# Optimization experiments

Measured on AMD Instinct MI355X. Metric: run time of the kernel, lower is better.

## Reference

```python
import jax, jax.numpy as jnp
import numpy as np

BN_EPS = 1e-5
ITER_N = 5

def _bn(x, gamma, beta, mean, var, axis):
    shape = [1] * x.ndim
    shape[axis] = -1
    r = lambda v: v.reshape(shape)
    return (x - r(mean)) * (r(gamma) / jnp.sqrt(r(var) + BN_EPS)) + r(beta)

def _covpool(x):
    # x: (B, d, M); MPNCOV CovpoolLayer: y = x @ I_hat @ x^T, I_hat = (1/M)I - (1/M^2)11^T
    M = x.shape[-1]
    I_hat = (-1.0 / (M * M)) * jnp.ones((M, M), x.dtype) + (1.0 / M) * jnp.eye(M, dtype=x.dtype)
    return jnp.einsum('bdm,mn,ben->bde', x, I_hat, x)

def _sqrtm_ns(A, iterN=ITER_N):
    # MPNCOV SqrtmLayer: trace-normalized Newton-Schulz iteration
    d = A.shape[-1]
    I3 = 3.0 * jnp.eye(d, dtype=A.dtype)
    normA = jnp.trace(A, axis1=1, axis2=2) / 3.0          # (B,)
    A_n = A / normA[:, None, None]
    ZY = 0.5 * (I3 - A_n)
    Y = A_n @ ZY
    Z = ZY
    for _ in range(iterN - 2):
        ZY = 0.5 * (I3 - Z @ Y)
        Y = Y @ ZY
        Z = ZY @ Z
    YZY = 0.5 * (Y @ (I3 - Z @ Y))
    return YZY * jnp.sqrt(normA)[:, None, None]

def setup_inputs() -> dict:
    key = jax.random.key(0)
    ks = jax.random.split(key, 12)
    B, C, H, W = 64, 1024, 16, 16
    D, R = 128, H * W  # att_dim, sp_reso
    return {
        'x': jax.random.normal(ks[0], (B, C, H, W), jnp.float32),
        'w_dr': jax.random.normal(ks[1], (D, C), jnp.float32) * 0.02,
        'b_dr': jax.random.normal(ks[2], (D,), jnp.float32) * 0.02,
        'bn1_gamma': jnp.ones((D,), jnp.float32),
        'bn1_beta': jnp.zeros((D,), jnp.float32),
        'bn1_mean': jax.random.normal(ks[3], (D,), jnp.float32) * 0.1,
        'bn1_var': jax.random.uniform(ks[4], (D,), jnp.float32, 0.5, 1.5),
        'bn2_gamma': jnp.ones((R,), jnp.float32),
        'bn2_beta': jnp.zeros((R,), jnp.float32),
        'bn2_mean': jax.random.normal(ks[5], (R,), jnp.float32) * 0.1,
        'bn2_var': jax.random.uniform(ks[6], (R,), jnp.float32, 0.5, 1.5),
        'rc_w': jax.random.normal(ks[7], (R,), jnp.float32) * 0.1 + 1.0,
        'rc_b': jax.random.normal(ks[8], (R,), jnp.float32) * 0.02,
        'fc_w': jax.random.normal(ks[9], (R, R * R), jnp.float32) * 0.004,
        'fc_b': jax.random.normal(ks[10], (R,), jnp.float32) * 0.02,
    }

def reference(x, w_dr, b_dr, bn1_gamma, bn1_beta, bn1_mean, bn1_var,
              bn2_gamma, bn2_beta, bn2_mean, bn2_var, rc_w, rc_b, fc_w, fc_b):
    B, C, H, W = x.shape
    # 1x1 dimension-reduction conv + BN + ReLU
    y = jnp.einsum('bchw,dc->bdhw', x, w_dr) + b_dr[None, :, None, None]
    y = jax.nn.relu(_bn(y, bn1_gamma, bn1_beta, bn1_mean, bn1_var, axis=1))
    # (B, D, HW) -> (B, HW, D): HW spatial positions as 'channels', D as samples
    y = y.reshape(B, -1, H * W).transpose(0, 2, 1)
    cov = _covpool(y)                  # (B, HW, HW)
    s = _sqrtm_ns(cov, ITER_N)         # (B, HW, HW)
    # row BN over first HW axis (channels of the (B, HW, HW, 1) view)
    s = _bn(s, bn2_gamma, bn2_beta, bn2_mean, bn2_var, axis=1)
    # grouped (depthwise) 1x1 row conv: per-row scale + bias
    s = s * rc_w[None, :, None] + rc_b[None, :, None]
    att = jax.nn.sigmoid(s.reshape(B, -1) @ fc_w.T + fc_b)   # (B, HW)
    att = att.reshape(B, 1, H, W)
    return x * att
```

## Files before the change

kernel.cpp:

```cpp
#include <hip/hip_runtime.h>

typedef unsigned short u16;
typedef unsigned int   u32;
typedef __attribute__((ext_vector_type(8))) short bf8;
typedef __attribute__((ext_vector_type(4))) float f4;
typedef __attribute__((ext_vector_type(16))) float f16f;

#define MFMA(a,b,c)   __builtin_amdgcn_mfma_f32_16x16x32_bf16(a,b,c,0,0,0)
#define MFMA32(a,b,c) __builtin_amdgcn_mfma_f32_32x32x16_bf16(a,b,c,0,0,0)

__device__ __forceinline__ u16 f2bf(float f){
  u32 u = __float_as_uint(f);
  u += 0x7fffu + ((u >> 16) & 1u);
  return (u16)(u >> 16);
}
__device__ __forceinline__ float bf2f(u16 h){ return __uint_as_float(((u32)h) << 16); }
__device__ __forceinline__ u32 pk2(float a, float b){ return (u32)f2bf(a) | ((u32)f2bf(b) << 16); }

__device__ __forceinline__ void glds16(const u16* g, u16* l){
  __builtin_amdgcn_global_load_lds((const __attribute__((address_space(1))) u32*)g,
                                   (__attribute__((address_space(3))) u32*)l, 16, 0, 0);
}

__device__ __forceinline__ bf8 ldsFrag(const char* m, int row0, int k0, int pitch){
  int l = threadIdx.x & 63;
  int r = row0 + (l & 15);
  int kb = ((k0 + ((l >> 4) << 3)) << 1) ^ ((r & 7) << 4);
  return *(const bf8*)(m + r * pitch + kb);
}
__device__ __forceinline__ void ldsPut(char* m, int row, int col, int pitch, u16 v){
  int kb = (col << 1) ^ ((row & 7) << 4);
  *(u16*)(m + row * pitch + kb) = v;
}

__device__ __forceinline__ bf8 fragNS(const char* m, int r0, int ks, int l){
  int r = r0 + (l & 31);
  int kb = ((ks << 5) + ((l >> 5) << 4)) ^ ((r & 15) << 4);
  return *(const bf8*)(m + r * 256 + kb);
}
__device__ __forceinline__ bf8 fragWT(const char* m, int r0, int ks, int l){
  int r = r0 + (l & 31);
  int kb = ((ks << 5) + ((l >> 5) << 4)) ^ ((r & 15) << 4);
  return *(const bf8*)(m + r * 512 + kb);
}
__device__ __forceinline__ char* nsAddr(char* m, int row, int col4){
  return m + row * 256 + ((col4 << 1) ^ ((row & 15) << 4));
}

__device__ __forceinline__ void mmPass(const char* A, const char* B, f16f (&acc)[2][2],
                                       int R0, int C0, int l){
  #pragma unroll
  for (int ks = 0; ks < 8; ++ks){
    bf8 a0 = fragNS(A, R0,      ks, l);
    bf8 a1 = fragNS(A, R0 + 32, ks, l);
    bf8 b0 = fragNS(B, C0,      ks, l);
    bf8 b1 = fragNS(B, C0 + 32, ks, l);
    acc[0][0] = MFMA32(a0, b0, acc[0][0]); acc[0][1] = MFMA32(a0, b1, acc[0][1]);
    acc[1][0] = MFMA32(a1, b0, acc[1][0]); acc[1][1] = MFMA32(a1, b1, acc[1][1]);
  }
}

__device__ __forceinline__ void writeTile(char* D, const f16f (&acc)[2][2], int R0, int C0, int l,
                                          float scale, float dval, const uint2* adv){
  #pragma unroll
  for (int ri = 0; ri < 2; ++ri)
  #pragma unroll
  for (int ci = 0; ci < 2; ++ci)
  #pragma unroll
  for (int g = 0; g < 4; ++g){
    int srow = C0 + ci * 32 + (l & 31);
    int scol = R0 + ri * 32 + g * 8 + ((l >> 5) << 2);
    float v[4];
    #pragma unroll
    for (int q = 0; q < 4; ++q){
      float x = scale * acc[ri][ci][g * 4 + q];
      x += ((scol + q) == srow) ? dval : 0.f;
      v[q] = x;
    }
    if (adv){
      uint2 ad = adv[(ri * 2 + ci) * 4 + g];
      v[0] += 1.5f * bf2f((u16)ad.x);
      v[1] += 1.5f * bf2f((u16)(ad.x >> 16));
      v[2] += 1.5f * bf2f((u16)ad.y);
      v[3] += 1.5f * bf2f((u16)(ad.y >> 16));
    }
    *(uint2*)nsAddr(D, srow, scol) = make_uint2(pk2(v[0], v[1]), pk2(v[2], v[3]));
  }
}

__global__ __launch_bounds__(256) void k_prep(const float* __restrict__ wdr,
                                              float* __restrict__ logits,
                                              u16* __restrict__ prep){
  int i = blockIdx.x * 256 + threadIdx.x;
  if (i < 16384) logits[i] = 0.f;
  #pragma unroll
  for (int j = 0; j < 2; ++j){
    int e = i + j * 65536;
    int chunk = e >> 13, rem = e & 8191, d = rem >> 6, cb2 = rem & 63;
    int c = ((cb2 * 2) ^ ((d & 7) << 4)) >> 1;
    prep[e] = f2bf(wdr[d * 1024 + chunk * 64 + c]);
  }
}

__global__ __launch_bounds__(512) void k_conv(
    const u16* __restrict__ wprep, const float* __restrict__ x, const float* __restrict__ bdr,
    const float* __restrict__ g1, const float* __restrict__ be1,
    const float* __restrict__ m1, const float* __restrict__ v1,
    u16* __restrict__ Wg, u16* __restrict__ WTg){
  __shared__ union {
    struct { u16 A[4][8192]; u16 Bt[2][2048]; } s;
    struct { float y[128 * 33]; float musum[512]; float mu[32]; } e;
  } sm;
  int t = threadIdx.x;
  int b = blockIdx.x >> 3, hw0 = (blockIdx.x & 7) * 32;
  const float* xb = x + (size_t)b * 262144 + hw0;

  int w = t >> 6, l = t & 63;
  int d0 = (w >> 1) * 32, hh = (w & 1) * 16;
  int lc = l & 15, lr = (l >> 4) * 4;

  const f4 fz = {0.f, 0.f, 0.f, 0.f};
  f4 acc[2]; acc[0] = fz; acc[1] = fz;

  int cp = t >> 5, hwl = t & 31;
  int bo0 = (4 * cp) ^ ((hwl & 7) << 4);
  int bo1 = (4 * cp + 64) ^ ((hwl & 7) << 4);

  float br[3][4];
  #pragma unroll
  for (int j = 0; j < 3; ++j){
    glds16(wprep + j * 8192 + t * 8,        sm.s.A[j] + t * 8);
    glds16(wprep + j * 8192 + 4096 + t * 8, sm.s.A[j] + 4096 + t * 8);
    __builtin_amdgcn_sched_barrier(0);
    int c0 = j * 64;
    br[j][0] = xb[(size_t)(c0 + 2 * cp)      * 256 + hwl];
    br[j][1] = xb[(size_t)(c0 + 2 * cp + 1)  * 256 + hwl];
    br[j][2] = xb[(size_t)(c0 + 2 * cp + 32) * 256 + hwl];
    br[j][3] = xb[(size_t)(c0 + 2 * cp + 33) * 256 + hwl];
    __builtin_amdgcn_sched_barrier(0);
  }

  #pragma unroll
  for (int k = 0; k < 16; ++k){
    if (k <= 12){
      const u16* src = wprep + (k + 3) * 8192;
      glds16(src + t * 8,        sm.s.A[(k + 3) & 3] + t * 8);
      glds16(src + 4096 + t * 8, sm.s.A[(k + 3) & 3] + 4096 + t * 8);
    }
    __builtin_amdgcn_sched_barrier(0);
    if (k <= 12)      asm volatile("s_waitcnt vmcnt(14)" ::: "memory");
    else if (k == 13) asm volatile("s_waitcnt vmcnt(12)" ::: "memory");
    else if (k == 14) asm volatile("s_waitcnt vmcnt(6)" ::: "memory");
    else              asm volatile("s_waitcnt vmcnt(0)" ::: "memory");
    __builtin_amdgcn_sched_barrier(0);
    *(u32*)((char*)sm.s.Bt[k & 1] + hwl * 128 + bo0) = pk2(br[k % 3][0], br[k % 3][1]);
    *(u32*)((char*)sm.s.Bt[k & 1] + hwl * 128 + bo1) = pk2(br[k % 3][2], br[k % 3][3]);
    __builtin_amdgcn_sched_barrier(0);
    if (k <= 12){
      int c0 = (k + 3) * 64;
      br[k % 3][0] = xb[(size_t)(c0 + 2 * cp)      * 256 + hwl];
      br[k % 3][1] = xb[(size_t)(c0 + 2 * cp + 1)  * 256 + hwl];
      br[k % 3][2] = xb[(size_t)(c0 + 2 * cp + 32) * 256 + hwl];
      br[k % 3][3] = xb[(size_t)(c0 + 2 * cp + 33) * 256 + hwl];
    }
    __builtin_amdgcn_sched_barrier(0);
    asm volatile("s_waitcnt lgkmcnt(0)" ::: "memory");
    __builtin_amdgcn_sched_barrier(0);
    __builtin_amdgcn_s_barrier();
    __builtin_amdgcn_sched_barrier(0);
    #pragma unroll
    for (int ks = 0; ks < 2; ++ks){
      int k0 = ks * 32;
      bf8 a0 = ldsFrag((const char*)sm.s.A[k & 3], d0,      k0, 128);
      bf8 a1 = ldsFrag((const char*)sm.s.A[k & 3], d0 + 16, k0, 128);
      bf8 b0 = ldsFrag((const char*)sm.s.Bt[k & 1], hh, k0, 128);
      acc[0] = MFMA(a0, b0, acc[0]);
      acc[1] = MFMA(a1, b0, acc[1]);
    }
    __builtin_amdgcn_sched_barrier(0);
    __builtin_amdgcn_s_barrier();
    __builtin_amdgcn_sched_barrier(0);
  }
  __syncthreads();

  #pragma unroll
  for (int i = 0; i < 2; ++i)
    #pragma unroll
    for (int r = 0; r < 4; ++r){
      int d = d0 + i * 16 + lr + r;
      float s1 = g1[d] * rsqrtf(v1[d] + 1e-5f);
      float t1 = (bdr[d] - m1[d]) * s1 + be1[d];
      int hwp = hh + lc;
      sm.e.y[d * 33 + hwp] = fmaxf(acc[i][r] * s1 + t1, 0.f);
    }
  __syncthreads();
  { int part = t >> 5, col = t & 31;
    float s = 0.f;
    #pragma unroll
    for (int i2 = 0; i2 < 8; ++i2) s += sm.e.y[(part * 8 + i2) * 33 + col];
    sm.e.musum[part * 32 + col] = s;
  }
  __syncthreads();
  if (t < 32){
    float m = 0.f;
    #pragma unroll
    for (int p = 0; p < 16; ++p) m += sm.e.musum[p * 32 + t];
    sm.e.mu[t] = m * (1.0f / 128.0f);
  }
  __syncthreads();
  const float ISM = 0.08838834764831845f;
  { int hwp = t >> 4, dc = (t & 15) * 8;
    float muv = sm.e.mu[hwp];
    u32 q[4];
    #pragma unroll
    for (int jj = 0; jj < 4; ++jj){
      float a = (sm.e.y[(dc + 2 * jj)     * 33 + hwp] - muv) * ISM;
      float c = (sm.e.y[(dc + 2 * jj + 1) * 33 + hwp] - muv) * ISM;
      q[jj] = pk2(a, c);
    }
    *(uint4*)(Wg + ((size_t)(b * 256 + hw0 + hwp) * 128 + dc)) = make_uint4(q[0], q[1], q[2], q[3]);
  }
  { int d = t >> 2, hc = (t & 3) * 8;
    u32 q[4];
    #pragma unroll
    for (int jj = 0; jj < 4; ++jj){
      int h0 = hc + 2 * jj, h1 = hc + 2 * jj + 1;
      float a = (sm.e.y[d * 33 + h0] - sm.e.mu[h0]) * ISM;
      float c = (sm.e.y[d * 33 + h1] - sm.e.mu[h1]) * ISM;
      q[jj] = pk2(a, c);
    }
    *(uint4*)(WTg + ((size_t)(b * 128 + d) * 256 + hw0 + hc)) = make_uint4(q[0], q[1], q[2], q[3]);
  }
}

extern __shared__ char smns[];
__global__ __launch_bounds__(512, 2) void k_ns(const u16* __restrict__ WT,
                                               u16* __restrict__ yf, float* __restrict__ normAg){
  int b = blockIdx.x, t = threadIdx.x;
  char* Yb = smns;
  char* Zb = smns + 32768;
  char* T1 = smns + 65536;
  char* T2 = smns + 98304;
  char* T3 = smns + 131072;
  char* WTl = smns + 65536;
  char* G   = T3;
  float* trp = (float*)smns;

  int w = t >> 6, l = t & 63;
  int wq = w & 3;
  int R0 = (wq >> 1) * 64, C0 = (wq & 1) * 64;

  { const u16* src = WT + (size_t)b * 32768;
    int row = t >> 2, q = t & 3;
    #pragma unroll
    for (int j = 0; j < 8; ++j) {
      int c16 = q + j * 4;
      bf8 v = *(const bf8*)(src + row * 256 + c16 * 8);
      int ph = c16 ^ (row & 15);
      *(bf8*)(WTl + row * 512 + ph * 16) = v;
    }
  }
  if (t == 0) *trp = 0.f;
  __syncthreads();

  int R0g = (w & 3) * 32, C0g = (w >> 2) * 64;
  const f16f fz16 = {};
  f16f gac[2]; gac[0] = fz16; gac[1] = fz16;
  #pragma unroll
  for (int ks = 0; ks < 16; ++ks){
    bf8 a  = fragWT(WTl, R0g,      ks, l);
    bf8 b0 = fragWT(WTl, C0g,      ks, l);
    bf8 b1 = fragWT(WTl, C0g + 32, ks, l);
    gac[0] = MFMA32(a, b0, gac[0]);
    gac[1] = MFMA32(a, b1, gac[1]);
  }
  float tp = 0.f;
  #pragma unroll
  for (int ci = 0; ci < 2; ++ci)
    #pragma unroll
    for (int e = 0; e < 16; ++e){
      int row = R0g + (e & 3) + 8 * (e >> 2) + ((l >> 5) << 2);
      int col = C0g + ci * 32 + (l & 31);
      if (row == col) tp += gac[ci][e];
    }
  #pragma unroll
  for (int off = 32; off > 0; off >>= 1) tp += __shfl_down(tp, off);
  if (l == 0) atomicAdd(trp, tp);
  __syncthreads();

  float normA = fmaxf(*trp / 3.0f, 1e-12f);
  if (t == 0) normAg[b] = normA;
  float inv = 1.0f / normA;
  #pragma unroll
  for (int ci = 0; ci < 2; ++ci)
    #pragma unroll
    for (int g = 0; g < 4; ++g){
      int srow = C0g + ci * 32 + (l & 31);
      int scol = R0g + g * 8 + ((l >> 5) << 2);
      float v0 = gac[ci][g * 4 + 0] * inv, v1 = gac[ci][g * 4 + 1] * inv;
      float v2 = gac[ci][g * 4 + 2] * inv, v3 = gac[ci][g * 4 + 3] * inv;
      *(uint2*)nsAddr(G, srow, scol) = make_uint2(pk2(v0, v1), pk2(v2, v3));
    }
  __syncthreads();

  bf8 gA[8], gB[8];
  #pragma unroll
  for (int ks = 0; ks < 8; ++ks){
    gA[ks] = fragNS(G, C0,      ks, l);
    gB[ks] = fragNS(G, C0 + 32, ks, l);
  }
  { int row = t >> 2, q4 = t & 3;
    #pragma unroll
    for (int j = 0; j < 4; ++j){
      int c16 = q4 * 4 + j;
      int ph = c16 ^ (row & 15);
      bf8 gg = *(const bf8*)(G + row * 256 + ph * 16);
      bf8 yv, zv;
      #pragma unroll
      for (int e = 0; e < 8; ++e){
        int col = c16 * 8 + e;
        float y = -0.5f * bf2f((u16)gg[e]) + ((col == row) ? 1.5f : 0.f);
        yv[e] = (short)f2bf(y);
        zv[e] = (col == row) ? (short)f2bf(-0.5f) : (short)0;
      }
      *(bf8*)(Yb + row * 256 + ph * 16) = yv;
      *(bf8*)(Zb + row * 256 + ph * 16) = zv;
    }
  }
  __syncthreads();

  float z0 = 1.5f;
  for (int it = 0; it < 4; ++it){
    {
      f16f acc[2][2]; acc[0][0] = fz16; acc[0][1] = fz16; acc[1][0] = fz16; acc[1][1] = fz16;
      const char* As = (w < 4) ? Zb : Yb;
      #pragma unroll
      for (int ks = 0; ks < 8; ++ks){
        bf8 a0 = fragNS(As, R0,      ks, l);
        bf8 a1 = fragNS(As, R0 + 32, ks, l);
        acc[0][0] = MFMA32(a0, gA[ks], acc[0][0]); acc[0][1] = MFMA32(a0, gB[ks], acc[0][1]);
        acc[1][0] = MFMA32(a1, gA[ks], acc[1][0]); acc[1][1] = MFMA32(a1, gB[ks], acc[1][1]);
      }
      writeTile((w < 4) ? T1 : T3, acc, R0, C0, l, 1.0f, (w < 4) ? z0 : 0.f, nullptr);
    }
    __syncthreads();

    uint2 adv[16];
    {
      const char* addsrc = (w < 4) ? Zb : Yb;
      #pragma unroll
      for (int ri = 0; ri < 2; ++ri)
      #pragma unroll
      for (int ci = 0; ci < 2; ++ci)
      #pragma unroll
      for (int g = 0; g < 4; ++g){
        int srow = C0 + ci * 32 + (l & 31);
        int scol = R0 + ri * 32 + g * 8 + ((l >> 5) << 2);
        adv[(ri * 2 + ci) * 4 + g] = *(const uint2*)nsAddr((char*)addsrc, srow, scol);
      }
      int hC0 = C0 + ((w >> 2) << 5);
      f16f a2[2]; a2[0] = fz16; a2[1] = fz16;
      #pragma unroll
      for (int ks = 0; ks < 8; ++ks){
        bf8 a0 = fragNS(T1, R0,      ks, l);
        bf8 a1 = fragNS(T1, R0 + 32, ks, l);
        bf8 b0 = fragNS(Yb, hC0,     ks, l);
        a2[0] = MFMA32(a0, b0, a2[0]);
        a2[1] = MFMA32(a1, b0, a2[1]);
      }
      #pragma unroll
      for (int ri = 0; ri < 2; ++ri)
      #pragma unroll
      for (int g = 0; g < 4; ++g){
        int srow = hC0 + (l & 31);
        int scol = R0 + ri * 32 + g * 8 + ((l >> 5) << 2);
        float v0 = -0.5f * a2[ri][g * 4 + 0], v1 = -0.5f * a2[ri][g * 4 + 1];
        float v2 = -0.5f * a2[ri][g * 4 + 2], v3 = -0.5f * a2[ri][g * 4 + 3];
        *(uint2*)nsAddr(T2, srow, scol) = make_uint2(pk2(v0, v1), pk2(v2, v3));
      }
    }
    __syncthreads();

    if ((w >= 4) || (it < 3)){
      f16f acc[2][2]; acc[0][0] = fz16; acc[0][1] = fz16; acc[1][0] = fz16; acc[1][1] = fz16;
      const char* A3 = (w < 4) ? T2 : T3;
      const char* B3 = (w < 4) ? T1 : T2;
      mmPass(A3, B3, acc, R0, C0, l);
      writeTile((w < 4) ? Zb : Yb, acc, R0, C0, l, 1.0f, 0.f, adv);
    }
    __syncthreads();
    z0 *= 1.5f;
  }

  { int row = t >> 2, q = t & 3;
    u16* dst = yf + (size_t)b * 16384 + row * 128;
    #pragma unroll
    for (int j = 0; j < 4; ++j) {
      int c16 = q * 4 + j;
      int ph = c16 ^ (row & 15);
      *(bf8*)(dst + c16 * 8) = *(const bf8*)(Yb + row * 256 + ph * 16);
    }
  }
}

extern __shared__ char smex[];
__global__ __launch_bounds__(512) void k_expand(
    const u16* __restrict__ Wg, const u16* __restrict__ yf, const float* __restrict__ normAg,
    const float* __restrict__ g2, const float* __restrict__ be2, const float* __restrict__ m2,
    const float* __restrict__ v2, const float* __restrict__ rcw, const float* __restrict__ rcb,
    u16* __restrict__ sp){
  int blk = blockIdx.x, b = blk >> 2, iband = blk & 3;
  char* Bm = smex;
  char* Yl = smex + 65536;
  char* El = smex + 98304;
  int t = threadIdx.x;
  { const u16* src = Wg + (size_t)b * 32768;
    int row = t >> 1, q = t & 1;
    #pragma unroll
    for (int j = 0; j < 8; ++j) {
      int c16 = q + j * 2;
      bf8 v = *(const bf8*)(src + row * 128 + c16 * 8);
      int ph = c16 ^ (row & 7);
      *(bf8*)(Bm + row * 256 + ph * 16) = v;
    } }
  { const u16* src = yf + (size_t)b * 16384;
    int row = t >> 2, q = t & 3;
    #pragma unroll
    for (int j = 0; j < 4; ++j) {
      int c16 = q + j * 4;
      bf8 v = *(const bf8*)(src + row * 128 + c16 * 8);
      int ph = c16 ^ (row & 7);
      *(bf8*)(Yl + row * 256 + ph * 16) = v;
    } }
  __syncthreads();
  int w = t >> 6, l = t & 63, lc = l & 15, lr = (l >> 4) * 4;
  const f4 fz = {0.f, 0.f, 0.f, 0.f};
  { int r0 = (w >> 2) * 32, c0 = (w & 3) * 32;
    f4 acc[2][2];
    acc[0][0] = fz; acc[0][1] = fz; acc[1][0] = fz; acc[1][1] = fz;
    #pragma unroll
    for (int kk = 0; kk < 4; ++kk) {
      int k0 = kk * 32;
      bf8 a0 = ldsFrag(Bm, iband * 64 + r0,      k0, 256);
      bf8 a1 = ldsFrag(Bm, iband * 64 + r0 + 16, k0, 256);
      bf8 b0 = ldsFrag(Yl, c0,      k0, 256);
      bf8 b1 = ldsFrag(Yl, c0 + 16, k0, 256);
      acc[0][0] = MFMA(a0, b0, acc[0][0]); acc[0][1] = MFMA(a0, b1, acc[0][1]);
      acc[1][0] = MFMA(a1, b0, acc[1][0]); acc[1][1] = MFMA(a1, b1, acc[1][1]);
    }
    #pragma unroll
    for (int i = 0; i < 2; ++i)
      #pragma unroll
      for (int j = 0; j < 2; ++j)
        #pragma unroll
        for (int r = 0; r < 4; ++r)
          ldsPut(El, r0 + i * 16 + lr + r, c0 + j * 16 + lc, 256, f2bf(acc[i][j][r]));
  }
  __syncthreads();
  { float invs = rsqrtf(normAg[b]);
    int r0 = (w >> 2) * 32, c0 = (w & 3) * 64;
    f4 acc[2][4];
    #pragma unroll
    for (int i = 0; i < 2; ++i)
      #pragma unroll
      for (int j = 0; j < 4; ++j) acc[i][j] = fz;
    #pragma unroll
    for (int kk = 0; kk < 4; ++kk) {
      int k0 = kk * 32;
      bf8 a0 = ldsFrag(El, r0,      k0, 256);
      bf8 a1 = ldsFrag(El, r0 + 16, k0, 256);
      bf8 b0 = ldsFrag(Bm, c0,      k0, 256);
      bf8 b1 = ldsFrag(Bm, c0 + 16, k0, 256);
      bf8 b2 = ldsFrag(Bm, c0 + 32, k0, 256);
      bf8 b3 = ldsFrag(Bm, c0 + 48, k0, 256);
      acc[0][0] = MFMA(a0, b0, acc[0][0]); acc[0][1] = MFMA(a0, b1, acc[0][1]);
      acc[0][2] = MFMA(a0, b2, acc[0][2]); acc[0][3] = MFMA(a0, b3, acc[0][3]);
      acc[1][0] = MFMA(a1, b0, acc[1][0]); acc[1][1] = MFMA(a1, b1, acc[1][1]);
      acc[1][2] = MFMA(a1, b2, acc[1][2]); acc[1][3] = MFMA(a1, b3, acc[1][3]);
    }
    #pragma unroll
    for (int i = 0; i < 2; ++i)
      #pragma unroll
      for (int r = 0; r < 4; ++r) {
        int il = r0 + i * 16 + lr + r;
        int ig = iband * 64 + il;
        float bs = g2[ig] * rsqrtf(v2[ig] + 1e-5f);
        float al = bs * rcw[ig];
        float be = (be2[ig] - m2[ig] * bs) * rcw[ig] + rcb[ig];
        #pragma unroll
        for (int j = 0; j < 4; ++j) {
          int jg = c0 + j * 16 + lc;
          sp[(size_t)b * 65536 + ig * 256 + jg] = f2bf(acc[i][j][r] * invs * al + be);
        }
      }
  }
}

__global__ __launch_bounds__(256, 5) void k_fc(const u16* __restrict__ sp,
                                               const float* __restrict__ fcw,
                                               float4* __restrict__ partial4){
  __shared__ char Bl[16384];
  int kc = blockIdx.x >> 2, rq = blockIdx.x & 3;
  int t = threadIdx.x, w = t >> 6, l = t & 63;
  int k0 = kc * 128, rbase = rq * 64;
  int br0 = (w & 1) * 32;
  int cr0 = (w >> 1) * 32;

  float4 fb[8];
  #pragma unroll
  for (int j = 0; j < 8; ++j){
    int fid = t + 256 * j;
    int row = fid >> 5, c4 = fid & 31;
    fb[j] = *(const float4*)(fcw + (size_t)(rbase + row) * 65536 + k0 + c4 * 4);
  }
  bf8 fa[8];
  #pragma unroll
  for (int g = 0; g < 2; ++g)
    #pragma unroll
    for (int ks = 0; ks < 4; ++ks)
      fa[g * 4 + ks] = *(const bf8*)(sp + (size_t)(br0 + 16 * g + (l & 15)) * 65536
                                     + k0 + ks * 32 + (l >> 4) * 8);
  #pragma unroll
  for (int j = 0; j < 8; ++j){
    int fid = t + 256 * j;
    int row = fid >> 5, c4 = fid & 31;
    int off = row * 256 + ((c4 * 8) ^ ((row & 7) << 4));
    *(uint2*)(Bl + off) = make_uint2(pk2(fb[j].x, fb[j].y), pk2(fb[j].z, fb[j].w));
  }
  __syncthreads();

  const f4 fz = {0.f, 0.f, 0.f, 0.f};
  f4 acc[2][2];
  acc[0][0] = fz; acc[0][1] = fz; acc[1][0] = fz; acc[1][1] = fz;
  #pragma unroll
  for (int ks = 0; ks < 4; ++ks){
    bf8 b0 = ldsFrag(Bl, cr0,      ks * 32, 256);
    bf8 b1 = ldsFrag(Bl, cr0 + 16, ks * 32, 256);
    acc[0][0] = MFMA(fa[ks],     b0, acc[0][0]);
    acc[0][1] = MFMA(fa[ks],     b1, acc[0][1]);
    acc[1][0] = MFMA(fa[4 + ks], b0, acc[1][0]);
    acc[1][1] = MFMA(fa[4 + ks], b1, acc[1][1]);
  }

  float4* pout = partial4 + (size_t)kc * 4096 + (size_t)(rq * 256 + t) * 4;
  #pragma unroll
  for (int g = 0; g < 2; ++g)
    #pragma unroll
    for (int j = 0; j < 2; ++j){
      f4 v = acc[g][j];
      pout[g * 2 + j] = make_float4(v[0], v[1], v[2], v[3]);
    }
}

__global__ __launch_bounds__(256) void k_red1(const float4* __restrict__ partial4,
                                              float4* __restrict__ p3){
  int b = blockIdx.x, t = threadIdx.x;
  int s = b >> 4;
  int c4 = ((b & 15) << 8) + t;
  float4 a0 = {0,0,0,0}, a1 = {0,0,0,0}, a2 = {0,0,0,0}, a3 = {0,0,0,0};
  #pragma unroll 2
  for (int j = 0; j < 32; j += 4){
    float4 v0 = partial4[(size_t)(s + (j + 0) * 16) * 4096 + c4];
    float4 v1 = partial4[(size_t)(s + (j + 1) * 16) * 4096 + c4];
    float4 v2 = partial4[(size_t)(s + (j + 2) * 16) * 4096 + c4];
    float4 v3 = partial4[(size_t)(s + (j + 3) * 16) * 4096 + c4];
    a0.x += v0.x; a0.y += v0.y; a0.z += v0.z; a0.w += v0.w;
    a1.x += v1.x; a1.y += v1.y; a1.z += v1.z; a1.w += v1.w;
    a2.x += v2.x; a2.y += v2.y; a2.z += v2.z; a2.w += v2.w;
    a3.x += v3.x; a3.y += v3.y; a3.z += v3.z; a3.w += v3.w;
  }
  float4 s4;
  s4.x = (a0.x + a1.x) + (a2.x + a3.x);
  s4.y = (a0.y + a1.y) + (a2.y + a3.y);
  s4.z = (a0.z + a1.z) + (a2.z + a3.z);
  s4.w = (a0.w + a1.w) + (a2.w + a3.w);
  p3[(size_t)s * 4096 + c4] = s4;
}

__global__ __launch_bounds__(256) void k_red2(const float4* __restrict__ p3,
                                              float* __restrict__ logits){
  int c4 = blockIdx.x * 256 + threadIdx.x;
  float4 a = {0,0,0,0};
  #pragma unroll
  for (int s = 0; s < 16; ++s){
    float4 v = p3[(size_t)s * 4096 + c4];
    a.x += v.x; a.y += v.y; a.z += v.z; a.w += v.w;
  }
  int rq = c4 >> 10, t = (c4 >> 2) & 255, gj = c4 & 3;
  int g = gj >> 1, j = gj & 1, w = t >> 6, l = t & 63;
  int brow0 = (w & 1) * 32 + g * 16 + ((l >> 4) << 2);
  int rcol  = rq * 64 + (w >> 1) * 32 + j * 16 + (l & 15);
  float* dst = logits + brow0 * 256 + rcol;
  dst[0]   = a.x;
  dst[256] = a.y;
  dst[512] = a.z;
  dst[768] = a.w;
}

__global__ __launch_bounds__(256) void k_mul(const float* __restrict__ x,
                                             const float* __restrict__ logits,
                                             const float* __restrict__ fcb,
                                             float* __restrict__ out, int n4){
  int i = blockIdx.x * 256 + threadIdx.x;
  int str = gridDim.x * 256;
  for (; i < n4; i += str) {
    int e = i << 2;
    int b = e >> 18;
    int hw = e & 255;
    float4 xv = ((const float4*)x)[i];
    float4 lg = *(const float4*)(logits + (b << 8) + hw);
    float4 fb = *(const float4*)(fcb + hw);
    float4 o;
    o.x = xv.x / (1.f + expf(-(lg.x + fb.x)));
    o.y = xv.y / (1.f + expf(-(lg.y + fb.y)));
    o.z = xv.z / (1.f + expf(-(lg.z + fb.z)));
    o.w = xv.w / (1.f + expf(-(lg.w + fb.w)));
    ((float4*)out)[i] = o;
  }
}

extern "C" void kernel_launch(void* const* d_in, const int* in_sizes, int n_in,
                              void* d_out, int out_size, void* d_ws, size_t ws_size,
                              hipStream_t stream){
  const float* x   = (const float*)d_in[0];
  const float* wdr = (const float*)d_in[1];
  const float* bdr = (const float*)d_in[2];
  const float* g1  = (const float*)d_in[3];
  const float* be1 = (const float*)d_in[4];
  const float* m1  = (const float*)d_in[5];
  const float* v1  = (const float*)d_in[6];
  const float* g2  = (const float*)d_in[7];
  const float* be2 = (const float*)d_in[8];
  const float* m2  = (const float*)d_in[9];
  const float* v2  = (const float*)d_in[10];
  const float* rcw = (const float*)d_in[11];
  const float* rcb = (const float*)d_in[12];
  const float* fcw = (const float*)d_in[13];
  const float* fcb = (const float*)d_in[14];
  float* out = (float*)d_out;
  char* ws = (char*)d_ws;
  u16*    Wg  = (u16*)(ws);
  u16*    WTg = (u16*)(ws + (4u  << 20));
  u16*    yfg = (u16*)(ws + (8u  << 20));
  float*  nAg = (float*)(ws + (10u << 20));
  u16*    wpr = (u16*)(ws + (10u << 20) + 4096);
  u16*    spg = (u16*)(ws + (11u << 20));
  float*  lgt = (float*)(ws + (20u << 20));
  float4* p3  = (float4*)(ws + (22u << 20));
  float4* prt = (float4*)(ws + (24u << 20));

  hipFuncSetAttribute((const void*)k_ns,     hipFuncAttributeMaxDynamicSharedMemorySize, 163840);
  hipFuncSetAttribute((const void*)k_expand, hipFuncAttributeMaxDynamicSharedMemorySize, 114688);

  k_prep  <<<256,  256, 0,      stream>>>(wdr, lgt, wpr);
  k_conv  <<<512,  512, 0,      stream>>>(wpr, x, bdr, g1, be1, m1, v1, Wg, WTg);
  k_ns    <<<64,   512, 163840, stream>>>(WTg, yfg, nAg);
  k_expand<<<256,  512, 114688, stream>>>(Wg, yfg, nAg, g2, be2, m2, v2, rcw, rcb, spg);
  k_fc    <<<2048, 256, 0,      stream>>>(spg, fcw, prt);
  k_red1  <<<256,  256, 0,      stream>>>(prt, p3);
  k_red2  <<<16,   256, 0,      stream>>>(p3, lgt);
  k_mul   <<<2048, 256, 0,      stream>>>(x, lgt, fcb, out, 4194304);
}
```

Before: 117.2 us.

## Restructure FC GEMM split-K into 16-row groups with looped k-slabs and single reduction

The FC kernel previously launched 2048 blocks, each covering 128 K-elements for 64 output rows, and a two-stage reduction over 512 partial slabs followed. Now 1024 blocks each loop over 1024 K-elements in 128-wide chunks for 16 output rows, staging both activation and weight tiles in swizzled LDS. This cuts the partial buffer to 64 slabs, so a single reduction kernel replaces two and one launch is removed. In exchange, each block reloads the full 64-row activation tile per chunk while using it for only 16 weight rows, which adds activation traffic. It also syncs twice per chunk with no prefetch overlap.

```diff
diff --git a/kernel.cpp b/kernel.cpp
--- a/kernel.cpp
+++ b/kernel.cpp
@@ -496,100 +496,68 @@
   }
 }
 
-__global__ __launch_bounds__(256, 5) void k_fc(const u16* __restrict__ sp,
-                                               const float* __restrict__ fcw,
-                                               float4* __restrict__ partial4){
-  __shared__ char Bl[16384];
-  int kc = blockIdx.x >> 2, rq = blockIdx.x & 3;
+__global__ __launch_bounds__(256) void k_fc(const u16* __restrict__ sp,
+                                            const float* __restrict__ fcw,
+                                            float4* __restrict__ partial4){
+  __shared__ char Asp[16384];
+  __shared__ char Bf[4096];
+  int rg = blockIdx.x & 15, kslab = blockIdx.x >> 4;
   int t = threadIdx.x, w = t >> 6, l = t & 63;
-  int k0 = kc * 128, rbase = rq * 64;
-  int br0 = (w & 1) * 32;
-  int cr0 = (w >> 1) * 32;
-
-  float4 fb[8];
-  #pragma unroll
-  for (int j = 0; j < 8; ++j){
-    int fid = t + 256 * j;
-    int row = fid >> 5, c4 = fid & 31;
-    fb[j] = *(const float4*)(fcw + (size_t)(rbase + row) * 65536 + k0 + c4 * 4);
-  }
-  bf8 fa[8];
-  #pragma unroll
-  for (int g = 0; g < 2; ++g)
-    #pragma unroll
-    for (int ks = 0; ks < 4; ++ks)
-      fa[g * 4 + ks] = *(const bf8*)(sp + (size_t)(br0 + 16 * g + (l & 15)) * 65536
-                                     + k0 + ks * 32 + (l >> 4) * 8);
-  #pragma unroll
-  for (int j = 0; j < 8; ++j){
-    int fid = t + 256 * j;
-    int row = fid >> 5, c4 = fid & 31;
-    int off = row * 256 + ((c4 * 8) ^ ((row & 7) << 4));
-    *(uint2*)(Bl + off) = make_uint2(pk2(fb[j].x, fb[j].y), pk2(fb[j].z, fb[j].w));
-  }
-  __syncthreads();
+  int kbase = kslab * 1024;
 
   const f4 fz = {0.f, 0.f, 0.f, 0.f};
-  f4 acc[2][2];
-  acc[0][0] = fz; acc[0][1] = fz; acc[1][0] = fz; acc[1][1] = fz;
-  #pragma unroll
-  for (int ks = 0; ks < 4; ++ks){
-    bf8 b0 = ldsFrag(Bl, cr0,      ks * 32, 256);
-    bf8 b1 = ldsFrag(Bl, cr0 + 16, ks * 32, 256);
-    acc[0][0] = MFMA(fa[ks],     b0, acc[0][0]);
-    acc[0][1] = MFMA(fa[ks],     b1, acc[0][1]);
-    acc[1][0] = MFMA(fa[4 + ks], b0, acc[1][0]);
-    acc[1][1] = MFMA(fa[4 + ks], b1, acc[1][1]);
-  }
-
-  float4* pout = partial4 + (size_t)kc * 4096 + (size_t)(rq * 256 + t) * 4;
-  #pragma unroll
-  for (int g = 0; g < 2; ++g)
-    #pragma unroll
-    for (int j = 0; j < 2; ++j){
-      f4 v = acc[g][j];
-      pout[g * 2 + j] = make_float4(v[0], v[1], v[2], v[3]);
-    }
-}
-
-__global__ __launch_bounds__(256) void k_red1(const float4* __restrict__ partial4,
-                                              float4* __restrict__ p3){
-  int b = blockIdx.x, t = threadIdx.x;
-  int s = b >> 4;
-  int c4 = ((b & 15) << 8) + t;
-  float4 a0 = {0,0,0,0}, a1 = {0,0,0,0}, a2 = {0,0,0,0}, a3 = {0,0,0,0};
-  #pragma unroll 2
-  for (int j = 0; j < 32; j += 4){
-    float4 v0 = partial4[(size_t)(s + (j + 0) * 16) * 4096 + c4];
-    float4 v1 = partial4[(size_t)(s + (j + 1) * 16) * 4096 + c4];
-    float4 v2 = partial4[(size_t)(s + (j + 2) * 16) * 4096 + c4];
-    float4 v3 = partial4[(size_t)(s + (j + 3) * 16) * 4096 + c4];
-    a0.x += v0.x; a0.y += v0.y; a0.z += v0.z; a0.w += v0.w;
-    a1.x += v1.x; a1.y += v1.y; a1.z += v1.z; a1.w += v1.w;
-    a2.x += v2.x; a2.y += v2.y; a2.z += v2.z; a2.w += v2.w;
-    a3.x += v3.x; a3.y += v3.y; a3.z += v3.z; a3.w += v3.w;
-  }
-  float4 s4;
-  s4.x = (a0.x + a1.x) + (a2.x + a3.x);
-  s4.y = (a0.y + a1.y) + (a2.y + a3.y);
-  s4.z = (a0.z + a1.z) + (a2.z + a3.z);
-  s4.w = (a0.w + a1.w) + (a2.w + a3.w);
-  p3[(size_t)s * 4096 + c4] = s4;
-}
-
-__global__ __launch_bounds__(256) void k_red2(const float4* __restrict__ p3,
-                                              float* __restrict__ logits){
-  int c4 = blockIdx.x * 256 + threadIdx.x;
+  f4 acc = fz;
+
+  int frow = t >> 4, fc4 = t & 15;
+  const float* fsrc = fcw + (size_t)(rg * 16 + frow) * 65536 + kbase;
+  int arow = t >> 2, aq = t & 3;
+  const u16* asrc = sp + (size_t)arow * 65536 + kbase;
+
+  for (int c = 0; c < 8; ++c){
+    int k0 = c * 128;
+    float4 v0 = *(const float4*)(fsrc + k0 + fc4 * 4);
+    float4 v1 = *(const float4*)(fsrc + k0 + (fc4 + 16) * 4);
+    bf8 av[4];
+    #pragma unroll
+    for (int j = 0; j < 4; ++j)
+      av[j] = *(const bf8*)(asrc + k0 + (aq * 4 + j) * 8);
+    {
+      int o0 = frow * 256 + (((fc4 >> 1) ^ (frow & 7)) << 4) + ((fc4 & 1) << 3);
+      *(uint2*)(Bf + o0) = make_uint2(pk2(v0.x, v0.y), pk2(v0.z, v0.w));
+      int c4b = fc4 + 16;
+      int o1 = frow * 256 + (((c4b >> 1) ^ (frow & 7)) << 4) + ((c4b & 1) << 3);
+      *(uint2*)(Bf + o1) = make_uint2(pk2(v1.x, v1.y), pk2(v1.z, v1.w));
+      #pragma unroll
+      for (int j = 0; j < 4; ++j){
+        int c16 = aq * 4 + j;
+        *(bf8*)(Asp + arow * 256 + ((c16 ^ (arow & 7)) << 4)) = av[j];
+      }
+    }
+    __syncthreads();
+    #pragma unroll
+    for (int ks = 0; ks < 4; ++ks){
+      bf8 a = ldsFrag(Asp, w * 16, ks * 32, 256);
+      bf8 b = ldsFrag(Bf, 0, ks * 32, 256);
+      acc = MFMA(a, b, acc);
+    }
+    __syncthreads();
+  }
+  partial4[(size_t)(kslab * 16 + rg) * 256 + t] = make_float4(acc[0], acc[1], acc[2], acc[3]);
+}
+
+__global__ __launch_bounds__(256) void k_red(const float4* __restrict__ partial4,
+                                             float* __restrict__ logits){
+  int rg = blockIdx.x;
+  int t = threadIdx.x;
   float4 a = {0,0,0,0};
-  #pragma unroll
-  for (int s = 0; s < 16; ++s){
-    float4 v = p3[(size_t)s * 4096 + c4];
+  #pragma unroll 8
+  for (int ks = 0; ks < 64; ++ks){
+    float4 v = partial4[(size_t)(ks * 16 + rg) * 256 + t];
     a.x += v.x; a.y += v.y; a.z += v.z; a.w += v.w;
   }
-  int rq = c4 >> 10, t = (c4 >> 2) & 255, gj = c4 & 3;
-  int g = gj >> 1, j = gj & 1, w = t >> 6, l = t & 63;
-  int brow0 = (w & 1) * 32 + g * 16 + ((l >> 4) << 2);
-  int rcol  = rq * 64 + (w >> 1) * 32 + j * 16 + (l & 15);
+  int w = t >> 6, l = t & 63;
+  int brow0 = w * 16 + ((l >> 4) << 2);
+  int rcol = rg * 16 + (l & 15);
   float* dst = logits + brow0 * 256 + rcol;
   dst[0]   = a.x;
   dst[256] = a.y;
@@ -646,7 +614,6 @@
   u16*    wpr = (u16*)(ws + (10u << 20) + 4096);
   u16*    spg = (u16*)(ws + (11u << 20));
   float*  lgt = (float*)(ws + (20u << 20));
-  float4* p3  = (float4*)(ws + (22u << 20));
   float4* prt = (float4*)(ws + (24u << 20));
 
   hipFuncSetAttribute((const void*)k_ns,     hipFuncAttributeMaxDynamicSharedMemorySize, 163840);
@@ -656,8 +623,7 @@
   k_conv  <<<512,  512, 0,      stream>>>(wpr, x, bdr, g1, be1, m1, v1, Wg, WTg);
   k_ns    <<<64,   512, 163840, stream>>>(WTg, yfg, nAg);
   k_expand<<<256,  512, 114688, stream>>>(Wg, yfg, nAg, g2, be2, m2, v2, rcw, rcb, spg);
-  k_fc    <<<2048, 256, 0,      stream>>>(spg, fcw, prt);
-  k_red1  <<<256,  256, 0,      stream>>>(prt, p3);
-  k_red2  <<<16,   256, 0,      stream>>>(p3, lgt);
+  k_fc    <<<1024, 256, 0,      stream>>>(spg, fcw, prt);
+  k_red   <<<16,   256, 0,      stream>>>(prt, lgt);
   k_mul   <<<2048, 256, 0,      stream>>>(x, lgt, fcb, out, 4194304);
 }
```

Measured after the change: 113.9 us. -2.8%, faster.
